# Performance work log

Measured on AMD Instinct MI355X. Metric: run time of the kernel, lower is better.

## Reference

```python
import jax, jax.numpy as jnp
import numpy as np

B, N, C, R = 4, 4096, 64, 16
EPS = 1e-12


def setup_inputs() -> dict:
    key = jax.random.key(0)
    k_x, k_w, k_u = jax.random.split(key, 3)
    x = jax.random.normal(k_x, (B, N, C), dtype=jnp.float32)
    W = jax.random.uniform(k_w, (B, N, N), dtype=jnp.float32)
    # lazily-initialized learnable low-rank factor U ~ 0.01 * randn(N, r)
    U = 0.01 * jax.random.normal(k_u, (N, R), dtype=jnp.float32)
    w_scale = jnp.asarray(1.0, dtype=jnp.float32)
    return {"x": x, "W": W, "U": U, "w_scale": w_scale}


def reference(x, W, U, w_scale):
    # symmetrize adjacency: W <- (W + W^T)/2
    Ws = 0.5 * (W + jnp.swapaxes(W, -1, -2))            # [B,N,N]
    # low-rank symmetric gate A = sigmoid(U U^T), shared over batch
    A = jax.nn.sigmoid(U @ U.T)                          # [N,N]
    K = Ws * A[None, :, :]                               # [B,N,N]
    # degree normalization K <- D^{-1/2} K D^{-1/2}
    # (diag_embed + two bmms in the original == row/col broadcast scaling)
    deg = jnp.maximum(K.sum(axis=-1), EPS)               # [B,N]
    d = jax.lax.rsqrt(deg)                               # [B,N]
    K = K * d[:, :, None] * d[:, None, :]                # [B,N,N]
    # coupling: w_scale * K @ x
    return w_scale * jnp.einsum('bnm,bmc->bnc', K, x)    # [B,N,C]
```

## Files before the change

### kernel.cpp

```cpp
#include <hip/hip_runtime.h>
#include <hip/hip_bf16.h>

#define B_ 4
#define N_ 4096
#define C_ 64
#define R_ 16
#define EPS_ 1e-12f

typedef __attribute__((ext_vector_type(8))) short bf16x8;
typedef __attribute__((ext_vector_type(4))) float f32x4;

static __device__ __forceinline__ unsigned short f2bf(float f) {
    unsigned int u = __float_as_uint(f);
    unsigned int r = (u + 0x7fffu + ((u >> 16) & 1u)) >> 16;
    return (unsigned short)r;
}
static __device__ __forceinline__ float bf2f(unsigned short us) {
    return __uint_as_float(((unsigned int)us) << 16);
}

__global__ __launch_bounds__(256) void k_pass1(
    const float* __restrict__ W, const float* __restrict__ U,
    unsigned short* __restrict__ K0, float* __restrict__ deg)
{
    const int tj = blockIdx.x, ti = blockIdx.y;
    if (ti > tj) return;
    const int I = ti * 64, J = tj * 64;
    const bool diag = (ti == tj);
    const int t = threadIdx.x;
    const int ii = t >> 2, g = t & 3, jjg = g * 16;

    __shared__ float UJ[64][17];
    __shared__ float Wc[64][65];
    __shared__ __align__(16) unsigned short K0s[64][72];

    {
        const float4 v = *(const float4*)(U + (size_t)(J + (t >> 2)) * R_ + (t & 3) * 4);
        UJ[t >> 2][(t & 3) * 4 + 0] = v.x;
        UJ[t >> 2][(t & 3) * 4 + 1] = v.y;
        UJ[t >> 2][(t & 3) * 4 + 2] = v.z;
        UJ[t >> 2][(t & 3) * 4 + 3] = v.w;
    }

    float4 wcv[4], wrv[4], wcvN[4], wrvN[4];
    #pragma unroll
    for (int k = 0; k < 4; k++) {
        const int idx = t + 256 * k, row = idx >> 4, c4 = idx & 15;
        wcv[k] = *(const float4*)(W + ((size_t)(0 * N_ + J + row)) * N_ + I + c4 * 4);
    }
    #pragma unroll
    for (int h = 0; h < 4; h++)
        wrv[h] = *(const float4*)(W + ((size_t)(0 * N_ + I + ii)) * N_ + J + jjg + 4 * h);

    float ui[16];
    {
        const float* up = U + (size_t)(I + ii) * R_;
        #pragma unroll
        for (int h = 0; h < 4; h++) {
            float4 v = *(const float4*)(up + 4 * h);
            ui[4*h] = v.x; ui[4*h+1] = v.y; ui[4*h+2] = v.z; ui[4*h+3] = v.w;
        }
    }
    __syncthreads();

    float a[16];
    #pragma unroll
    for (int q = 0; q < 16; q++) {
        float s = 0.f;
        #pragma unroll
        for (int k = 0; k < 16; k++) s += ui[k] * UJ[jjg + q][k];
        a[q] = 1.0f / (1.0f + __expf(-s));
    }

    #pragma unroll
    for (int k = 0; k < 4; k++) {
        const int idx = t + 256 * k, row = idx >> 4, c4 = idx & 15;
        Wc[row][c4*4+0] = wcv[k].x; Wc[row][c4*4+1] = wcv[k].y;
        Wc[row][c4*4+2] = wcv[k].z; Wc[row][c4*4+3] = wcv[k].w;
    }
    __syncthreads();

    for (int b = 0; b < B_; b++) {
        if (b < B_ - 1) {
            #pragma unroll
            for (int k = 0; k < 4; k++) {
                const int idx = t + 256 * k, row = idx >> 4, c4 = idx & 15;
                wcvN[k] = *(const float4*)(W + ((size_t)((b+1) * N_ + J + row)) * N_ + I + c4 * 4);
            }
            #pragma unroll
            for (int h = 0; h < 4; h++)
                wrvN[h] = *(const float4*)(W + ((size_t)((b+1) * N_ + I + ii)) * N_ + J + jjg + 4 * h);
        }

        const float* wrf = (const float*)wrv;
        float sumI = 0.f;
        unsigned int pk[8];
        #pragma unroll
        for (int q = 0; q < 16; q++) {
            float k0 = 0.5f * (wrf[q] + Wc[jjg + q][ii]) * a[q];
            sumI += k0;
            unsigned short us = f2bf(k0);
            if (q & 1) pk[q >> 1] |= ((unsigned int)us) << 16;
            else       pk[q >> 1] = us;
        }
        *(int4*)(&K0s[ii][jjg])     = make_int4(pk[0], pk[1], pk[2], pk[3]);
        *(int4*)(&K0s[ii][jjg + 8]) = make_int4(pk[4], pk[5], pk[6], pk[7]);
        {
            unsigned short* dst = K0 + ((size_t)(b * N_ + I + ii)) * N_ + J + jjg;
            *(int4*)(dst)     = make_int4(pk[0], pk[1], pk[2], pk[3]);
            *(int4*)(dst + 8) = make_int4(pk[4], pk[5], pk[6], pk[7]);
        }
        {
            float s = sumI + __shfl_xor(sumI, 1, 64);
            s += __shfl_xor(s, 2, 64);
            if (g == 0) atomicAdd(deg + b * N_ + I + ii, s);
        }
        __syncthreads();

        if (!diag) {
            const int c2 = t & 31, r8 = t >> 5;
            unsigned int v[8];
            float cs0 = 0.f, cs1 = 0.f;
            #pragma unroll
            for (int k = 0; k < 8; k++) {
                v[k] = *(const unsigned int*)(&K0s[r8 * 8 + k][c2 * 2]);
                cs0 += bf2f((unsigned short)(v[k] & 0xffffu));
                cs1 += bf2f((unsigned short)(v[k] >> 16));
            }
            unsigned int plo[4], phi[4];
            #pragma unroll
            for (int m = 0; m < 4; m++) {
                plo[m] = (v[2*m] & 0xffffu) | (v[2*m+1] << 16);
                phi[m] = (v[2*m] >> 16) | (v[2*m+1] & 0xffff0000u);
            }
            unsigned short* dst0 = K0 + ((size_t)(b * N_ + J + 2 * c2)) * N_ + I + r8 * 8;
            unsigned short* dst1 = dst0 + N_;
            *(int4*)dst0 = make_int4(plo[0], plo[1], plo[2], plo[3]);
            *(int4*)dst1 = make_int4(phi[0], phi[1], phi[2], phi[3]);
            cs0 += __shfl_xor(cs0, 32, 64);
            cs1 += __shfl_xor(cs1, 32, 64);
            if ((t & 32) == 0) {
                atomicAdd(deg + b * N_ + J + 2 * c2,     cs0);
                atomicAdd(deg + b * N_ + J + 2 * c2 + 1, cs1);
            }
        }
        if (b < B_ - 1) {
            #pragma unroll
            for (int k = 0; k < 4; k++) {
                const int idx = t + 256 * k, row = idx >> 4, c4 = idx & 15;
                Wc[row][c4*4+0] = wcvN[k].x; Wc[row][c4*4+1] = wcvN[k].y;
                Wc[row][c4*4+2] = wcvN[k].z; Wc[row][c4*4+3] = wcvN[k].w;
            }
            #pragma unroll
            for (int h = 0; h < 4; h++) wrv[h] = wrvN[h];
            __syncthreads();
        }
    }
}

__global__ __launch_bounds__(256) void k_xdT(
    const float* __restrict__ x, const float* __restrict__ deg,
    unsigned short* __restrict__ xdT)
{
    const int jt = blockIdx.x, b = blockIdx.y;
    const int J = jt * 64, t = threadIdx.x;
    __shared__ float xt[64][69];
    #pragma unroll
    for (int k = 0; k < 4; k++) {
        int idx = t + 256 * k;
        int row = idx >> 4, f4 = idx & 15;
        float d = rsqrtf(fmaxf(deg[b * N_ + J + row], EPS_));
        float4 v = *(const float4*)(x + ((size_t)(b * N_ + J + row)) * C_ + f4 * 4);
        xt[row][f4*4+0] = v.x * d; xt[row][f4*4+1] = v.y * d;
        xt[row][f4*4+2] = v.z * d; xt[row][f4*4+3] = v.w * d;
    }
    __syncthreads();
    const int c = t >> 2, jg = (t & 3) * 16;
    unsigned int pk[8];
    #pragma unroll
    for (int q = 0; q < 16; q++) {
        unsigned short us = f2bf(xt[jg + q][c]);
        if (q & 1) pk[q >> 1] |= ((unsigned int)us) << 16;
        else       pk[q >> 1] = us;
    }
    unsigned short* dst = xdT + ((size_t)(b * C_ + c)) * N_ + J + jg;
    *(int4*)(dst)     = make_int4(pk[0], pk[1], pk[2], pk[3]);
    *(int4*)(dst + 8) = make_int4(pk[4], pk[5], pk[6], pk[7]);
}

__global__ __launch_bounds__(256) void k_gemm(
    const unsigned short* __restrict__ K0, const unsigned short* __restrict__ xdT,
    const float* __restrict__ deg, const float* __restrict__ wsc_p,
    float* __restrict__ out)
{
    const int rb = blockIdx.x, b = blockIdx.y;
    const int I = rb * 16;
    const int t = threadIdx.x, l = t & 63, w = t >> 6;
    const int fr = l & 15, fq = l >> 4, cw = w * 16;

    const unsigned short* Ap = K0  + ((size_t)(b * N_ + I + fr)) * N_ + fq * 8;
    const unsigned short* Bp = xdT + ((size_t)(b * C_ + cw + fr)) * N_ + fq * 8;

    f32x4 acc0 = {0.f, 0.f, 0.f, 0.f}, acc1 = {0.f, 0.f, 0.f, 0.f};
    #pragma unroll 8
    for (int k = 0; k < N_; k += 64) {
        bf16x8 a0 = *(const bf16x8*)(Ap + k);
        bf16x8 b0 = *(const bf16x8*)(Bp + k);
        bf16x8 a1 = *(const bf16x8*)(Ap + k + 32);
        bf16x8 b1 = *(const bf16x8*)(Bp + k + 32);
        acc0 = __builtin_amdgcn_mfma_f32_16x16x32_bf16(a0, b0, acc0, 0, 0, 0);
        acc1 = __builtin_amdgcn_mfma_f32_16x16x32_bf16(a1, b1, acc1, 0, 0, 0);
    }
    f32x4 acc = acc0 + acc1;

    const float wsc = wsc_p[0];
    #pragma unroll
    for (int r = 0; r < 4; r++) {
        const int row = I + fq * 4 + r;
        const float sc = wsc * rsqrtf(fmaxf(deg[b * N_ + row], EPS_));
        out[((size_t)(b * N_ + row)) * C_ + cw + fr] = sc * acc[r];
    }
}

extern "C" void kernel_launch(void* const* d_in, const int* in_sizes, int n_in,
                              void* d_out, int out_size, void* d_ws, size_t ws_size,
                              hipStream_t stream)
{
    const float* x   = (const float*)d_in[0];
    const float* W   = (const float*)d_in[1];
    const float* U   = (const float*)d_in[2];
    const float* wsc = (const float*)d_in[3];
    float* out = (float*)d_out;

    unsigned short* K0  = (unsigned short*)d_ws;
    float*          deg = (float*)((char*)d_ws + (size_t)B_ * N_ * N_ * 2);
    unsigned short* xdT = (unsigned short*)((char*)deg + (size_t)B_ * N_ * 4);

    hipMemsetAsync(deg, 0, (size_t)B_ * N_ * sizeof(float), stream);
    hipLaunchKernelGGL(k_pass1, dim3(64, 64), dim3(256), 0, stream, W, U, K0, deg);
    hipLaunchKernelGGL(k_xdT,  dim3(64, 4),   dim3(256), 0, stream, x, deg, xdT);
    hipLaunchKernelGGL(k_gemm, dim3(256, 4),  dim3(256), 0, stream, K0, xdT, deg, wsc, out);
}
```

Measured before the change: 522.1 us.

## Store K0 and xdT in MFMA fragment order and retile GEMM per wave

K0 and the scaled transposed x are now written in a pre-swizzled layout that matches the MFMA 16x16x32 operand fragments, so each wave in the GEMM reads one contiguous 1KB chunk per k-step instead of strided row segments. The GEMM is reorganised so each wave owns a 16-row tile and all 64 output columns with four accumulators, reusing one A fragment across four MFMAs. This quarters the number of blocks and cuts redundant A loads, at the cost of more scattered stores in pass1 and less grid parallelism in the GEMM.

```diff
diff --git a/kernel.cpp b/kernel.cpp
--- a/kernel.cpp
+++ b/kernel.cpp
@@ -17,6 +17,10 @@
 }
 static __device__ __forceinline__ float bf2f(unsigned short us) {
     return __uint_as_float(((unsigned int)us) << 16);
+}
+
+static __device__ __forceinline__ size_t k0f_off(int b, int rt, int k32, int fq, int fr) {
+    return ((((size_t)(b * 256 + rt)) * 128 + k32) * 4 + fq) * 128 + fr * 8;
 }
 
 __global__ __launch_bounds__(256) void k_pass1(
@@ -106,9 +110,11 @@
         *(int4*)(&K0s[ii][jjg])     = make_int4(pk[0], pk[1], pk[2], pk[3]);
         *(int4*)(&K0s[ii][jjg + 8]) = make_int4(pk[4], pk[5], pk[6], pk[7]);
         {
-            unsigned short* dst = K0 + ((size_t)(b * N_ + I + ii)) * N_ + J + jjg;
-            *(int4*)(dst)     = make_int4(pk[0], pk[1], pk[2], pk[3]);
-            *(int4*)(dst + 8) = make_int4(pk[4], pk[5], pk[6], pk[7]);
+            const int rt  = (I + ii) >> 4, fr = ii & 15;
+            const int k32 = (J >> 5) + (g >> 1), fqa = (g & 1) * 2;
+            unsigned short* dst = K0 + k0f_off(b, rt, k32, fqa, fr);
+            *(int4*)(dst)       = make_int4(pk[0], pk[1], pk[2], pk[3]);
+            *(int4*)(dst + 128) = make_int4(pk[4], pk[5], pk[6], pk[7]);
         }
         {
             float s = sumI + __shfl_xor(sumI, 1, 64);
@@ -133,10 +139,11 @@
                 plo[m] = (v[2*m] & 0xffffu) | (v[2*m+1] << 16);
                 phi[m] = (v[2*m] >> 16) | (v[2*m+1] & 0xffff0000u);
             }
-            unsigned short* dst0 = K0 + ((size_t)(b * N_ + J + 2 * c2)) * N_ + I + r8 * 8;
-            unsigned short* dst1 = dst0 + N_;
-            *(int4*)dst0 = make_int4(plo[0], plo[1], plo[2], plo[3]);
-            *(int4*)dst1 = make_int4(phi[0], phi[1], phi[2], phi[3]);
+            const int rtp  = (J >> 4) + (c2 >> 3), fr0 = (2 * c2) & 15;
+            const int k32p = (I >> 5) + (r8 >> 2), fqp = r8 & 3;
+            unsigned short* dst0 = K0 + k0f_off(b, rtp, k32p, fqp, fr0);
+            *(int4*)(dst0)     = make_int4(plo[0], plo[1], plo[2], plo[3]);
+            *(int4*)(dst0 + 8) = make_int4(phi[0], phi[1], phi[2], phi[3]);
             cs0 += __shfl_xor(cs0, 32, 64);
             cs1 += __shfl_xor(cs1, 32, 64);
             if ((t & 32) == 0) {
@@ -175,17 +182,23 @@
         xt[row][f4*4+2] = v.z * d; xt[row][f4*4+3] = v.w * d;
     }
     __syncthreads();
-    const int c = t >> 2, jg = (t & 3) * 16;
-    unsigned int pk[8];
-    #pragma unroll
-    for (int q = 0; q < 16; q++) {
-        unsigned short us = f2bf(xt[jg + q][c]);
-        if (q & 1) pk[q >> 1] |= ((unsigned int)us) << 16;
-        else       pk[q >> 1] = us;
-    }
-    unsigned short* dst = xdT + ((size_t)(b * C_ + c)) * N_ + J + jg;
-    *(int4*)(dst)     = make_int4(pk[0], pk[1], pk[2], pk[3]);
-    *(int4*)(dst + 8) = make_int4(pk[4], pk[5], pk[6], pk[7]);
+    #pragma unroll
+    for (int p = 0; p < 2; p++) {
+        const int linear = p * 256 + t;
+        const int k32h = linear >> 8, rem = linear & 255;
+        const int cg = rem >> 6, l = rem & 63, fq = l >> 4, fr = l & 15;
+        const int c = cg * 16 + fr;
+        const int jb = k32h * 32 + fq * 8;
+        unsigned int pk[4];
+        #pragma unroll
+        for (int m = 0; m < 4; m++) {
+            pk[m] = (unsigned int)f2bf(xt[jb + 2*m][c]) |
+                    ((unsigned int)f2bf(xt[jb + 2*m + 1][c]) << 16);
+        }
+        unsigned short* dst = xdT +
+            (((size_t)(b * 128 + (J >> 5) + k32h)) * 4 + cg) * 512 + l * 8;
+        *(int4*)dst = make_int4(pk[0], pk[1], pk[2], pk[3]);
+    }
 }
 
 __global__ __launch_bounds__(256) void k_gemm(
@@ -194,31 +207,39 @@
     float* __restrict__ out)
 {
     const int rb = blockIdx.x, b = blockIdx.y;
-    const int I = rb * 16;
     const int t = threadIdx.x, l = t & 63, w = t >> 6;
-    const int fr = l & 15, fq = l >> 4, cw = w * 16;
-
-    const unsigned short* Ap = K0  + ((size_t)(b * N_ + I + fr)) * N_ + fq * 8;
-    const unsigned short* Bp = xdT + ((size_t)(b * C_ + cw + fr)) * N_ + fq * 8;
-
-    f32x4 acc0 = {0.f, 0.f, 0.f, 0.f}, acc1 = {0.f, 0.f, 0.f, 0.f};
-    #pragma unroll 8
-    for (int k = 0; k < N_; k += 64) {
-        bf16x8 a0 = *(const bf16x8*)(Ap + k);
-        bf16x8 b0 = *(const bf16x8*)(Bp + k);
-        bf16x8 a1 = *(const bf16x8*)(Ap + k + 32);
-        bf16x8 b1 = *(const bf16x8*)(Bp + k + 32);
-        acc0 = __builtin_amdgcn_mfma_f32_16x16x32_bf16(a0, b0, acc0, 0, 0, 0);
-        acc1 = __builtin_amdgcn_mfma_f32_16x16x32_bf16(a1, b1, acc1, 0, 0, 0);
-    }
-    f32x4 acc = acc0 + acc1;
-
+    const int rt = rb * 4 + w;
+
+    const unsigned short* Ap = K0  + (size_t)(b * 256 + rt) * 65536 + l * 8;
+    const unsigned short* Bp = xdT + (size_t)b * 262144 + l * 8;
+
+    f32x4 acc0 = {0.f,0.f,0.f,0.f}, acc1 = {0.f,0.f,0.f,0.f};
+    f32x4 acc2 = {0.f,0.f,0.f,0.f}, acc3 = {0.f,0.f,0.f,0.f};
+
+    #pragma unroll 4
+    for (int k32 = 0; k32 < 128; k32++) {
+        bf16x8 av = *(const bf16x8*)(Ap + (size_t)k32 * 512);
+        bf16x8 b0 = *(const bf16x8*)(Bp + (size_t)k32 * 2048);
+        bf16x8 b1 = *(const bf16x8*)(Bp + (size_t)k32 * 2048 + 512);
+        bf16x8 b2 = *(const bf16x8*)(Bp + (size_t)k32 * 2048 + 1024);
+        bf16x8 b3 = *(const bf16x8*)(Bp + (size_t)k32 * 2048 + 1536);
+        acc0 = __builtin_amdgcn_mfma_f32_16x16x32_bf16(av, b0, acc0, 0, 0, 0);
+        acc1 = __builtin_amdgcn_mfma_f32_16x16x32_bf16(av, b1, acc1, 0, 0, 0);
+        acc2 = __builtin_amdgcn_mfma_f32_16x16x32_bf16(av, b2, acc2, 0, 0, 0);
+        acc3 = __builtin_amdgcn_mfma_f32_16x16x32_bf16(av, b3, acc3, 0, 0, 0);
+    }
+
+    const int fr = l & 15, fq = l >> 4;
     const float wsc = wsc_p[0];
     #pragma unroll
     for (int r = 0; r < 4; r++) {
-        const int row = I + fq * 4 + r;
+        const int row = rt * 16 + fq * 4 + r;
         const float sc = wsc * rsqrtf(fmaxf(deg[b * N_ + row], EPS_));
-        out[((size_t)(b * N_ + row)) * C_ + cw + fr] = sc * acc[r];
+        float* op = out + ((size_t)(b * N_ + row)) * C_;
+        op[fr]      = sc * acc0[r];
+        op[16 + fr] = sc * acc1[r];
+        op[32 + fr] = sc * acc2[r];
+        op[48 + fr] = sc * acc3[r];
     }
 }
 
@@ -238,6 +259,6 @@
 
     hipMemsetAsync(deg, 0, (size_t)B_ * N_ * sizeof(float), stream);
     hipLaunchKernelGGL(k_pass1, dim3(64, 64), dim3(256), 0, stream, W, U, K0, deg);
-    hipLaunchKernelGGL(k_xdT,  dim3(64, 4),   dim3(256), 0, stream, x, deg, xdT);
-    hipLaunchKernelGGL(k_gemm, dim3(256, 4),  dim3(256), 0, stream, K0, xdT, deg, wsc, out);
-}
+    hipLaunchKernelGGL(k_xdT,  dim3(64, 4),  dim3(256), 0, stream, x, deg, xdT);
+    hipLaunchKernelGGL(k_gemm, dim3(64, 4),  dim3(256), 0, stream, K0, xdT, deg, wsc, out);
+}
```

Measured after the change: 463.5 us. 11.2% less time.
